# Kernel optimization log

Measured on AMD Instinct MI355X. Metric: run time of the kernel, lower is better.

Reference implementation:

```python
import jax, jax.numpy as jnp
import numpy as np

NUM_OPS, B, T, D = 8, 8, 512, 1024


def setup_inputs() -> dict:
    key = jax.random.key(0)
    k1, k2, k3, k4 = jax.random.split(key, 4)
    x = jax.random.normal(k1, (B, T, D), dtype=jnp.float32)
    W = jax.random.normal(k2, (NUM_OPS, D, D), dtype=jnp.float32) * 0.02
    b = jnp.zeros((NUM_OPS, D), dtype=jnp.float32)
    logits = 0.001 * jax.random.normal(k3, (NUM_OPS,), dtype=jnp.float32)
    # uniform noise for Gumbel sampling (matches tf.random.uniform in sample_without_replacement)
    u = jax.random.uniform(k4, (NUM_OPS,), dtype=jnp.float32, minval=1e-6, maxval=1.0 - 1e-6)
    return {"x": x, "W": W, "b": b, "logits": logits, "u": u}


def reference(x, W, b, logits, u):
    # weights = softmax(logits); gumbel top-1 over log(weights) == log_softmax(logits)
    gumbel = -jnp.log(-jnp.log(u))
    idx = jnp.argmax(jax.nn.log_softmax(logits) + gumbel)
    # forward of ops_times_mask_binary: sum over ON ops (num_on_samples=1 -> single op)
    out = jnp.einsum('btd,de->bte', x, W[idx]) + b[idx]  # [B,T,D]
    return out
```

## Files before the change

kernel.cpp:

```cpp
#include <hip/hip_runtime.h>

typedef unsigned short u16;
typedef unsigned int u32;
typedef __attribute__((ext_vector_type(8))) short bf16x8;
typedef __attribute__((ext_vector_type(4))) float f32x4;

#define NUM_OPS 8
#define M_DIM 4096
#define K_DIM 1024
#define N_DIM 1024
#define KT 32


__device__ __forceinline__ u16 f2b(float f) {
  union { float f; u32 u; } v; v.f = f;
  u32 r = v.u + 0x7fffu + ((v.u >> 16) & 1u);
  return (u16)(r >> 16);
}

__device__ __forceinline__ u32 pk2(float a, float b) {
  return (u32)f2b(a) | ((u32)f2b(b) << 16);
}

__device__ __forceinline__ int compute_idx(const float* __restrict__ logits,
                                           const float* __restrict__ u) {
  int best = 0; float bv = -3.4e38f;
#pragma unroll
  for (int i = 0; i < NUM_OPS; ++i) {
    float v = logits[i] - logf(-logf(u[i]));
    if (v > bv) { bv = v; best = i; }
  }
  return best;
}

__global__ void prep_kernel(const float* __restrict__ x, const float* __restrict__ W,
                            const float* __restrict__ logits, const float* __restrict__ u,
                            u16* __restrict__ xb, u16* __restrict__ wt) {
  const int tid = threadIdx.x;
  const int bid = blockIdx.x;
  if (bid < 2048) {
    const int chunk = bid * 4 + (tid >> 6), l = tid & 63;
    const int mtile = chunk >> 5, ktile = chunk & 31;
    const float* src = x + (size_t)(mtile * 16 + (l & 15)) * K_DIM
                         + ktile * 32 + (l >> 4) * 8;
    float4 f0 = *(const float4*)(src);
    float4 f1 = *(const float4*)(src + 4);
    uint4 p;
    p.x = pk2(f0.x, f0.y); p.y = pk2(f0.z, f0.w);
    p.z = pk2(f1.x, f1.y); p.w = pk2(f1.z, f1.w);
    *(uint4*)(xb + (size_t)chunk * 512 + l * 8) = p;
  } else {
    __shared__ u16 t[64][66];
    const int wb = bid - 2048;
    const int kt = wb >> 4, nt = wb & 15;
    const int idx = compute_idx(logits, u);
    const float* Wi = W + (size_t)idx * K_DIM * N_DIM;
#pragma unroll
    for (int it = 0; it < 16; ++it) {
      int i = it * 256 + tid;
      int r = i >> 6, c = i & 63;
      t[r][c] = f2b(Wi[(size_t)(kt * 64 + r) * N_DIM + nt * 64 + c]);
    }
    __syncthreads();
#pragma unroll
    for (int it = 0; it < 2; ++it) {
      int s = it * 256 + tid;
      int c = s >> 6, l = s & 63;
      int ntl = c & 3, ktl = c >> 2;
      int kb = ktl * 32 + (l >> 4) * 8, nn = ntl * 16 + (l & 15);
      uint4 p;
      p.x = (u32)t[kb + 0][nn] | ((u32)t[kb + 1][nn] << 16);
      p.y = (u32)t[kb + 2][nn] | ((u32)t[kb + 3][nn] << 16);
      p.z = (u32)t[kb + 4][nn] | ((u32)t[kb + 5][nn] << 16);
      p.w = (u32)t[kb + 6][nn] | ((u32)t[kb + 7][nn] << 16);
      int chunk = (nt * 4 + ntl) * 32 + (kt * 2 + ktl);
      *(uint4*)(wt + (size_t)chunk * 512 + l * 8) = p;
    }
  }
}

__global__ __launch_bounds__(256) void gemm_kernel(
    const u16* __restrict__ xb, const u16* __restrict__ wt,
    const float* __restrict__ bvec, const float* __restrict__ logits,
    const float* __restrict__ u, float* __restrict__ out) {
  const int tid = threadIdx.x;
  const int w = tid >> 6, L = tid & 63;
  const int bid = blockIdx.x;
  const int x7 = bid & 7, r = bid >> 3;
  const int mt = x7 * 8 + (r >> 2);
  const int nt = (r & 3) * 4 + w;

  const u16* pa[4];
  const u16* pb[4];
#pragma unroll
  for (int f = 0; f < 4; ++f) {
    pa[f] = xb + ((size_t)(mt * 4 + f) * 32) * 512 + L * 8;
    pb[f] = wt + ((size_t)(nt * 4 + f) * 32) * 512 + L * 8;
  }

  f32x4 acc[4][4] = {};
  bf16x8 af[2][4], bf[2][4];

#pragma unroll
  for (int f = 0; f < 4; ++f) {
    af[0][f] = *(const bf16x8*)(pa[f]);
    bf[0][f] = *(const bf16x8*)(pb[f]);
  }

#pragma unroll
  for (int kt = 0; kt < KT; ++kt) {
    const int cur = kt & 1, nxt = cur ^ 1;
    if (kt + 1 < KT) {
      const int ko = (kt + 1) * 512;
#pragma unroll
      for (int f = 0; f < 4; ++f) {
        af[nxt][f] = *(const bf16x8*)(pa[f] + ko);
        bf[nxt][f] = *(const bf16x8*)(pb[f] + ko);
      }
    }
#pragma unroll
    for (int mf = 0; mf < 4; ++mf)
#pragma unroll
      for (int nf = 0; nf < 4; ++nf)
        acc[mf][nf] = __builtin_amdgcn_mfma_f32_16x16x32_bf16(
            af[cur][mf], bf[cur][nf], acc[mf][nf], 0, 0, 0);
  }

  const int idx = compute_idx(logits, u);
  const float* bi = bvec + (size_t)idx * N_DIM;
#pragma unroll
  for (int mf = 0; mf < 4; ++mf) {
    int row = mt * 64 + 16 * mf + (L >> 4) * 4;
#pragma unroll
    for (int nf = 0; nf < 4; ++nf) {
      int col = nt * 64 + 16 * nf + (L & 15);
      float bv = bi[col];
#pragma unroll
      for (int rr = 0; rr < 4; ++rr)
        out[(size_t)(row + rr) * N_DIM + col] = acc[mf][nf][rr] + bv;
    }
  }
}


extern "C" void kernel_launch(void* const* d_in, const int* in_sizes, int n_in,
                              void* d_out, int out_size, void* d_ws, size_t ws_size,
                              hipStream_t stream) {
  const float* x      = (const float*)d_in[0];
  const float* W      = (const float*)d_in[1];
  const float* bvec   = (const float*)d_in[2];
  const float* logits = (const float*)d_in[3];
  const float* u      = (const float*)d_in[4];
  float* out = (float*)d_out;

  u16* xb = (u16*)d_ws;
  u16* wt = (u16*)d_ws + (size_t)M_DIM * K_DIM;

  prep_kernel<<<2048 + 256, 256, 0, stream>>>(x, W, logits, u, xb, wt);
  gemm_kernel<<<256, 256, 0, stream>>>(xb, wt, bvec, logits, u, out);
}
```

Before: 122.7 us.

## Split K across wave pairs with LDS reduction and deepen register prefetch

Each 64x64 output tile is now computed by two waves that each cover half of K, and the halves are combined through shared memory before the bias add and store. The grid doubles to 512 blocks so more waves are resident to hide global-load latency, and the register prefetch goes from double to triple buffering. The cost is extra LDS traffic, a block barrier, and higher register pressure under the tighter launch bounds.

```diff
diff --git a/kernel.cpp b/kernel.cpp
--- a/kernel.cpp
+++ b/kernel.cpp
@@ -9,7 +9,7 @@
 #define M_DIM 4096
 #define K_DIM 1024
 #define N_DIM 1024
-#define KT 32
+#define KT_PER_WAVE 16
 
 
 __device__ __forceinline__ u16 f2b(float f) {
@@ -79,43 +79,55 @@
   }
 }
 
-__global__ __launch_bounds__(256) void gemm_kernel(
+__global__ __launch_bounds__(256, 2) void gemm_kernel(
     const u16* __restrict__ xb, const u16* __restrict__ wt,
     const float* __restrict__ bvec, const float* __restrict__ logits,
     const float* __restrict__ u, float* __restrict__ out) {
+  __shared__ f32x4 xc[2 * 1024];
+
   const int tid = threadIdx.x;
   const int w = tid >> 6, L = tid & 63;
   const int bid = blockIdx.x;
-  const int x7 = bid & 7, r = bid >> 3;
-  const int mt = x7 * 8 + (r >> 2);
-  const int nt = (r & 3) * 4 + w;
+  const int x7 = bid & 7, t = bid >> 3;
+  const int tl = w >> 1;
+  const int ti = t * 2 + tl;
+  const int mt = x7 * 8 + (ti >> 4);
+  const int nt = ti & 15;
+  const int kh = w & 1;
+  const int k0 = kh * KT_PER_WAVE;
 
   const u16* pa[4];
   const u16* pb[4];
 #pragma unroll
   for (int f = 0; f < 4; ++f) {
-    pa[f] = xb + ((size_t)(mt * 4 + f) * 32) * 512 + L * 8;
-    pb[f] = wt + ((size_t)(nt * 4 + f) * 32) * 512 + L * 8;
+    pa[f] = xb + ((size_t)((mt * 4 + f) * 32 + k0)) * 512 + L * 8;
+    pb[f] = wt + ((size_t)((nt * 4 + f) * 32 + k0)) * 512 + L * 8;
   }
 
   f32x4 acc[4][4] = {};
-  bf16x8 af[2][4], bf[2][4];
+  bf16x8 af[3][4], bf[3][4];
 
 #pragma unroll
   for (int f = 0; f < 4; ++f) {
     af[0][f] = *(const bf16x8*)(pa[f]);
     bf[0][f] = *(const bf16x8*)(pb[f]);
   }
+#pragma unroll
+  for (int f = 0; f < 4; ++f) {
+    af[1][f] = *(const bf16x8*)(pa[f] + 512);
+    bf[1][f] = *(const bf16x8*)(pb[f] + 512);
+  }
 
 #pragma unroll
-  for (int kt = 0; kt < KT; ++kt) {
-    const int cur = kt & 1, nxt = cur ^ 1;
-    if (kt + 1 < KT) {
-      const int ko = (kt + 1) * 512;
+  for (int kt = 0; kt < KT_PER_WAVE; ++kt) {
+    const int cur = kt % 3;
+    if (kt + 2 < KT_PER_WAVE) {
+      const int nb_ = (kt + 2) % 3;
+      const int ko = (kt + 2) * 512;
 #pragma unroll
       for (int f = 0; f < 4; ++f) {
-        af[nxt][f] = *(const bf16x8*)(pa[f] + ko);
-        bf[nxt][f] = *(const bf16x8*)(pb[f] + ko);
+        af[nb_][f] = *(const bf16x8*)(pa[f] + ko);
+        bf[nb_][f] = *(const bf16x8*)(pb[f] + ko);
       }
     }
 #pragma unroll
@@ -126,18 +138,29 @@
             af[cur][mf], bf[cur][nf], acc[mf][nf], 0, 0, 0);
   }
 
-  const int idx = compute_idx(logits, u);
-  const float* bi = bvec + (size_t)idx * N_DIM;
+  if (kh == 1) {
 #pragma unroll
-  for (int mf = 0; mf < 4; ++mf) {
-    int row = mt * 64 + 16 * mf + (L >> 4) * 4;
+    for (int mf = 0; mf < 4; ++mf)
 #pragma unroll
-    for (int nf = 0; nf < 4; ++nf) {
-      int col = nt * 64 + 16 * nf + (L & 15);
-      float bv = bi[col];
+      for (int nf = 0; nf < 4; ++nf)
+        xc[tl * 1024 + (mf * 4 + nf) * 64 + L] = acc[mf][nf];
+  }
+  __syncthreads();
+  if (kh == 0) {
+    const int idx = compute_idx(logits, u);
+    const float* bi = bvec + (size_t)idx * N_DIM;
 #pragma unroll
-      for (int rr = 0; rr < 4; ++rr)
-        out[(size_t)(row + rr) * N_DIM + col] = acc[mf][nf][rr] + bv;
+    for (int mf = 0; mf < 4; ++mf) {
+      int row = mt * 64 + 16 * mf + (L >> 4) * 4;
+#pragma unroll
+      for (int nf = 0; nf < 4; ++nf) {
+        int col = nt * 64 + 16 * nf + (L & 15);
+        float bv = bi[col];
+        f32x4 o = acc[mf][nf] + xc[tl * 1024 + (mf * 4 + nf) * 64 + L];
+#pragma unroll
+        for (int r = 0; r < 4; ++r)
+          out[(size_t)(row + r) * N_DIM + col] = o[r] + bv;
+      }
     }
   }
 }
@@ -157,5 +180,5 @@
   u16* wt = (u16*)d_ws + (size_t)M_DIM * K_DIM;
 
   prep_kernel<<<2048 + 256, 256, 0, stream>>>(x, W, logits, u, xb, wt);
-  gemm_kernel<<<256, 256, 0, stream>>>(xb, wt, bvec, logits, u, out);
+  gemm_kernel<<<512, 256, 0, stream>>>(xb, wt, bvec, logits, u, out);
 }
```

New measurement: 114.2 us. -6.9%, faster.
